# Kernel optimization log

Measured on AMD Instinct MI355X. Metric: run time of the kernel, lower is better.

Reference implementation:

```python
import jax, jax.numpy as jnp
import numpy as np

# --- sampler hyperparameters (from init_kwargs) ---
NUM_SAMPLES = 8
NUM_EXP = 256
OVER_SAMPLE_RATE = 1.5
NUM_SAMPLES_BOUNDARY = 40
DTIME_MAX = 5.0
NUM_EVENT_TYPES = 20
NUM_MARK = 10
B, S = 32, 512


def _intensity(event_seq, sample_times, emb, scale, bias):
    """Synthetic multivariate intensity: [B,S,N] times -> [B,S,N,NUM_MARK]."""
    e = emb[event_seq]  # [B,S,M] gather by event type (irregular access)
    return jax.nn.softplus(e[:, :, None, :] + scale * jnp.cos(sample_times)[..., None] + bias)


def setup_inputs() -> dict:
    key = jax.random.key(0)
    ks = jax.random.split(key, 6)
    dt = jax.random.uniform(ks[0], (B, S), dtype=jnp.float32) + 1e-3  # positive deltas
    t = jnp.cumsum(dt, axis=1)  # monotone timestamps
    ev = jax.random.randint(ks[1], (B, S), 0, NUM_EVENT_TYPES, dtype=jnp.int64)
    # raw Exp(1) draws (inverse-CDF of uniform)
    u = jax.random.uniform(ks[2], (B, S, NUM_EXP), dtype=jnp.float32, minval=1e-7, maxval=1.0)
    exp_raw = -jnp.log(u)
    unif = jax.random.uniform(ks[3], (B, S, NUM_SAMPLES, NUM_EXP), dtype=jnp.float32)
    emb = jax.random.normal(ks[4], (NUM_EVENT_TYPES, NUM_MARK), dtype=jnp.float32)
    scale = jax.random.normal(ks[5], (NUM_MARK,), dtype=jnp.float32) * 0.5
    bias = jnp.zeros((NUM_MARK,), dtype=jnp.float32)
    return {"time_seq": t, "time_delta_seq": dt, "event_seq": ev,
            "exp_raw": exp_raw, "unif_numbers": unif,
            "emb": emb, "scale": scale, "bias": bias}


def reference(time_seq, time_delta_seq, event_seq, exp_raw, unif_numbers, emb, scale, bias):
    # --- compute_intensity_upper_bound (compute_last_step_only=False) ---
    lin = jnp.linspace(0.0, 1.0, NUM_SAMPLES_BOUNDARY, dtype=jnp.float32)  # [K]
    t_bound = time_seq[:, :, None] + time_delta_seq[:, :, None] * lin[None, None, :]  # [B,S,K]
    lam_bound = _intensity(event_seq, t_bound, emb, scale, bias)  # [B,S,K,M]
    upper = jnp.max(lam_bound.sum(-1), axis=-1) * OVER_SAMPLE_RATE  # [B,S]

    # --- sample_exp_distribution ---
    exp_numbers = exp_raw / upper[:, :, None]  # [B,S,E]

    # --- intensities at sampled times ---
    time_exp = time_seq[:, :, None] + exp_numbers  # [B,S,E]
    total_int = _intensity(event_seq, time_exp, emb, scale, bias).sum(-1)  # [B,S,E]

    # --- sample_accept (broadcast instead of tile) ---
    criterion = unif_numbers * upper[:, :, None, None] / total_int[:, :, None, :]  # [B,S,NS,E]
    accept = criterion < 1.0
    masked_exp = jnp.where(accept, exp_numbers[:, :, None, :], jnp.inf)
    min_time = jnp.min(masked_exp, axis=3)  # [B,S,NS] first-accepted = smallest accepted dt
    res = jnp.where(jnp.isinf(min_time), jnp.float32(DTIME_MAX), min_time)
    res = jnp.minimum(res, 1e5)
    weights = jnp.ones_like(res) / res.shape[2]
    return res, weights
```

## Files before the change

kernel.cpp:

```cpp
#include <hip/hip_runtime.h>
#include <math.h>

#define NBATCH 32
#define NSEQ 512
#define NSAMP 8
#define NEXP 256
#define KBOUND 40
#define NMARK 10
#define DTIME_MAX 5.0f
#define OVER_SAMPLE 1.5f

__device__ __forceinline__ float fast_cos(float x) {
    constexpr double inv2pi_d = 0.15915494309189535;
    constexpr float chi = (float)inv2pi_d;
    constexpr float clo = (float)(inv2pi_d - (double)chi);
    float n = rintf(x * chi);
    float f = fmaf(x, chi, -n);
    f = fmaf(x, clo, f);
    return __builtin_amdgcn_cosf(f);
}

__device__ __forceinline__ float intensity_sum(float c, const float eb[NMARK],
                                               const float sc[NMARK]) {
    const float NLOG2E = -1.4426950408889634f;
    const float LN2    =  0.69314718055994531f;
    float acc0 = 0.f, acc1 = 0.f, p0 = 1.f, p1 = 1.f;
    #pragma unroll
    for (int m = 0; m < NMARK; m += 2) {
        float x0 = fmaf(sc[m],     c, eb[m]);
        float x1 = fmaf(sc[m + 1], c, eb[m + 1]);
        float e0 = __builtin_amdgcn_exp2f(fabsf(x0) * NLOG2E);
        float e1 = __builtin_amdgcn_exp2f(fabsf(x1) * NLOG2E);
        p0 *= (1.f + e0);
        p1 *= (1.f + e1);
        acc0 += fmaxf(x0, 0.f);
        acc1 += fmaxf(x1, 0.f);
    }
    return fmaf(LN2, __builtin_amdgcn_logf(p0 * p1), acc0 + acc1);
}

__global__ __launch_bounds__(256) void syn_event_sampler(
    const float* __restrict__ time_seq,
    const float* __restrict__ dt_seq,
    const int*   __restrict__ event_seq,
    const float* __restrict__ exp_raw,
    const float* __restrict__ unif,
    const float* __restrict__ emb,
    const float* __restrict__ scale,
    const float* __restrict__ bias,
    float* __restrict__ out_res,
    float* __restrict__ out_w)
{
    const int bs   = blockIdx.x;
    const int tid  = threadIdx.x;
    const int lane = tid & 63;
    const int wv   = tid >> 6;

    __shared__ float s_eb[NMARK], s_sc[NMARK];
    __shared__ float s_bmax[4];
    __shared__ float s_red[4][NSAMP];

    if (tid < NMARK) {
        int ev = event_seq[bs];
        s_eb[tid] = emb[ev * NMARK + tid] + bias[tid];
        s_sc[tid] = scale[tid];
    }
    __syncthreads();

    float eb[NMARK], sc[NMARK];
    #pragma unroll
    for (int m = 0; m < NMARK; ++m) { eb[m] = s_eb[m]; sc[m] = s_sc[m]; }

    const float t   = time_seq[bs];
    const float dtv = dt_seq[bs];

    float bsum = -INFINITY;
    if (lane < 10) {
        int k = wv * 10 + lane;
        const float step = 1.0f / 39.0f;
        float tb = __fadd_rn(t, __fmul_rn(dtv, __fmul_rn((float)k, step)));
        bsum = intensity_sum(fast_cos(tb), eb, sc);
    }
    #pragma unroll
    for (int off = 1; off < 64; off <<= 1)
        bsum = fmaxf(bsum, __shfl_xor(bsum, off, 64));
    if (lane == 0) s_bmax[wv] = bsum;
    __syncthreads();
    const float upper =
        fmaxf(fmaxf(s_bmax[0], s_bmax[1]), fmaxf(s_bmax[2], s_bmax[3])) * OVER_SAMPLE;

    const float eraw  = exp_raw[(size_t)bs * NEXP + tid];
    const float expn  = eraw / upper;
    const float total = intensity_sum(fast_cos(t + expn), eb, sc);

    const float* up = unif + (size_t)bs * NSAMP * NEXP + tid;
    float cand[NSAMP];
    #pragma unroll
    for (int ns = 0; ns < NSAMP; ++ns) {
        float u = up[(size_t)ns * NEXP];
        cand[ns] = (__fmul_rn(u, upper) < total) ? expn : INFINITY;
    }
    #pragma unroll
    for (int ns = 0; ns < NSAMP; ++ns) {
        float v = cand[ns];
        #pragma unroll
        for (int off = 1; off < 64; off <<= 1)
            v = fminf(v, __shfl_xor(v, off, 64));
        if (lane == 0) s_red[wv][ns] = v;
    }
    __syncthreads();

    if (tid < NSAMP) {
        float m0 = fminf(fminf(s_red[0][tid], s_red[1][tid]),
                         fminf(s_red[2][tid], s_red[3][tid]));
        float r = isinf(m0) ? DTIME_MAX : m0;
        r = fminf(r, 1e5f);
        out_res[(size_t)bs * NSAMP + tid] = r;
        out_w  [(size_t)bs * NSAMP + tid] = 1.0f / NSAMP;
    }
}

extern "C" void kernel_launch(void* const* d_in, const int* in_sizes, int n_in,
                              void* d_out, int out_size, void* d_ws, size_t ws_size,
                              hipStream_t stream) {
    const float* time_seq = (const float*)d_in[0];
    const float* dt_seq   = (const float*)d_in[1];
    const int*   ev_seq   = (const int*)  d_in[2];
    const float* exp_raw  = (const float*)d_in[3];
    const float* unif     = (const float*)d_in[4];
    const float* emb      = (const float*)d_in[5];
    const float* scale    = (const float*)d_in[6];
    const float* bias     = (const float*)d_in[7];

    float* out_res = (float*)d_out;
    float* out_w   = out_res + (size_t)NBATCH * NSEQ * NSAMP;

    dim3 grid(NBATCH * NSEQ);
    dim3 block(NEXP);
    syn_event_sampler<<<grid, block, 0, stream>>>(
        time_seq, dt_seq, ev_seq, exp_raw, unif, emb, scale, bias, out_res, out_w);
}
```

Before: 217.4 us.

## Map one wavefront per sequence position with float4 loads and no LDS syncs

Each 64-lane wavefront now handles a whole (batch, position) row, so each lane processes four exponential draws through float4 loads. The upper-bound reduction and the min reductions become wave-local shuffles, which removes the shared memory and all block-level barriers. Scalar inputs are broadcast with readfirstlane, and the uniform loads are issued early so they overlap the bound computation. In exchange each lane carries more registers (32 unif values plus four totals), which could lower occupancy.

```diff
diff --git a/kernel.cpp b/kernel.cpp
--- a/kernel.cpp
+++ b/kernel.cpp
@@ -39,6 +39,10 @@
     return fmaf(LN2, __builtin_amdgcn_logf(p0 * p1), acc0 + acc1);
 }
 
+__device__ __forceinline__ float rfl_f(float x) {
+    return __int_as_float(__builtin_amdgcn_readfirstlane(__float_as_int(x)));
+}
+
 __global__ __launch_bounds__(256) void syn_event_sampler(
     const float* __restrict__ time_seq,
     const float* __restrict__ dt_seq,
@@ -51,72 +55,70 @@
     float* __restrict__ out_res,
     float* __restrict__ out_w)
 {
-    const int bs   = blockIdx.x;
-    const int tid  = threadIdx.x;
-    const int lane = tid & 63;
-    const int wv   = tid >> 6;
+    const int lane = threadIdx.x & 63;
+    const int wv   = threadIdx.x >> 6;
+    const int bs   = blockIdx.x * 4 + wv;
 
-    __shared__ float s_eb[NMARK], s_sc[NMARK];
-    __shared__ float s_bmax[4];
-    __shared__ float s_red[4][NSAMP];
+    const float4 er4 = *reinterpret_cast<const float4*>(
+        exp_raw + (size_t)bs * NEXP + 4 * lane);
+    const float* ub = unif + (size_t)bs * NSAMP * NEXP + 4 * lane;
+    float4 u4[NSAMP];
+    #pragma unroll
+    for (int ns = 0; ns < NSAMP; ++ns)
+        u4[ns] = *reinterpret_cast<const float4*>(ub + (size_t)ns * NEXP);
 
-    if (tid < NMARK) {
-        int ev = event_seq[bs];
-        s_eb[tid] = emb[ev * NMARK + tid] + bias[tid];
-        s_sc[tid] = scale[tid];
-    }
-    __syncthreads();
+    const float t   = rfl_f(time_seq[bs]);
+    const float dtv = rfl_f(dt_seq[bs]);
+    const int   ev  = __builtin_amdgcn_readfirstlane(event_seq[bs]);
 
     float eb[NMARK], sc[NMARK];
     #pragma unroll
-    for (int m = 0; m < NMARK; ++m) { eb[m] = s_eb[m]; sc[m] = s_sc[m]; }
-
-    const float t   = time_seq[bs];
-    const float dtv = dt_seq[bs];
+    for (int m = 0; m < NMARK; ++m) {
+        eb[m] = emb[ev * NMARK + m] + bias[m];
+        sc[m] = scale[m];
+    }
 
     float bsum = -INFINITY;
-    if (lane < 10) {
-        int k = wv * 10 + lane;
+    if (lane < KBOUND) {
         const float step = 1.0f / 39.0f;
-        float tb = __fadd_rn(t, __fmul_rn(dtv, __fmul_rn((float)k, step)));
+        float tb = __fadd_rn(t, __fmul_rn(dtv, __fmul_rn((float)lane, step)));
         bsum = intensity_sum(fast_cos(tb), eb, sc);
     }
     #pragma unroll
     for (int off = 1; off < 64; off <<= 1)
         bsum = fmaxf(bsum, __shfl_xor(bsum, off, 64));
-    if (lane == 0) s_bmax[wv] = bsum;
-    __syncthreads();
-    const float upper =
-        fmaxf(fmaxf(s_bmax[0], s_bmax[1]), fmaxf(s_bmax[2], s_bmax[3])) * OVER_SAMPLE;
+    const float upper = bsum * OVER_SAMPLE;
 
-    const float eraw  = exp_raw[(size_t)bs * NEXP + tid];
-    const float expn  = eraw / upper;
-    const float total = intensity_sum(fast_cos(t + expn), eb, sc);
+    float expn[4], total[4];
+    expn[0] = er4.x / upper;  expn[1] = er4.y / upper;
+    expn[2] = er4.z / upper;  expn[3] = er4.w / upper;
+    #pragma unroll
+    for (int i = 0; i < 4; ++i)
+        total[i] = intensity_sum(fast_cos(t + expn[i]), eb, sc);
 
-    const float* up = unif + (size_t)bs * NSAMP * NEXP + tid;
-    float cand[NSAMP];
+    float vmin[NSAMP];
     #pragma unroll
     for (int ns = 0; ns < NSAMP; ++ns) {
-        float u = up[(size_t)ns * NEXP];
-        cand[ns] = (__fmul_rn(u, upper) < total) ? expn : INFINITY;
-    }
-    #pragma unroll
-    for (int ns = 0; ns < NSAMP; ++ns) {
-        float v = cand[ns];
+        float c0 = (__fmul_rn(u4[ns].x, upper) < total[0]) ? expn[0] : INFINITY;
+        float c1 = (__fmul_rn(u4[ns].y, upper) < total[1]) ? expn[1] : INFINITY;
+        float c2 = (__fmul_rn(u4[ns].z, upper) < total[2]) ? expn[2] : INFINITY;
+        float c3 = (__fmul_rn(u4[ns].w, upper) < total[3]) ? expn[3] : INFINITY;
+        float v = fminf(fminf(c0, c1), fminf(c2, c3));
         #pragma unroll
         for (int off = 1; off < 64; off <<= 1)
             v = fminf(v, __shfl_xor(v, off, 64));
-        if (lane == 0) s_red[wv][ns] = v;
+        vmin[ns] = v;
     }
-    __syncthreads();
 
-    if (tid < NSAMP) {
-        float m0 = fminf(fminf(s_red[0][tid], s_red[1][tid]),
-                         fminf(s_red[2][tid], s_red[3][tid]));
-        float r = isinf(m0) ? DTIME_MAX : m0;
+    float rv = vmin[0];
+    #pragma unroll
+    for (int ns = 1; ns < NSAMP; ++ns)
+        rv = (lane == ns) ? vmin[ns] : rv;
+    if (lane < NSAMP) {
+        float r = isinf(rv) ? DTIME_MAX : rv;
         r = fminf(r, 1e5f);
-        out_res[(size_t)bs * NSAMP + tid] = r;
-        out_w  [(size_t)bs * NSAMP + tid] = 1.0f / NSAMP;
+        out_res[(size_t)bs * NSAMP + lane] = r;
+        out_w  [(size_t)bs * NSAMP + lane] = 1.0f / NSAMP;
     }
 }
 
@@ -135,8 +137,8 @@
     float* out_res = (float*)d_out;
     float* out_w   = out_res + (size_t)NBATCH * NSEQ * NSAMP;
 
-    dim3 grid(NBATCH * NSEQ);
-    dim3 block(NEXP);
+    dim3 grid((NBATCH * NSEQ) / 4);
+    dim3 block(256);
     syn_event_sampler<<<grid, block, 0, stream>>>(
         time_seq, dt_seq, ev_seq, exp_raw, unif, emb, scale, bias, out_res, out_w);
 }
```

New measurement: 213.9 us. Within noise of the previous version (-1.6%).
